# Kernel optimization log

Hardware: AMD Instinct MI355X
Metric: run time of the kernel (lower is better)

Reference implementation:

```python
import jax, jax.numpy as jnp
import numpy as np


def setup_inputs() -> dict:
    key = jax.random.key(0)
    kx, ky = jax.random.split(key)
    x = jax.random.normal(kx, (4, 8192, 3), dtype=jnp.float32)
    y = jax.random.normal(ky, (4, 8192, 3), dtype=jnp.float32)
    return {"x": x, "y": y}


def _chamfer(x, y):
    # x: [B, N, D], y: [B, M, D]
    x2 = jnp.sum(x * x, axis=-1)                      # [B, N]
    y2 = jnp.sum(y * y, axis=-1)                      # [B, M]
    xy = jnp.einsum("bnd,bmd->bnm", x, y)             # [B, N, M]
    d2 = x2[:, :, None] + y2[:, None, :] - 2.0 * xy   # [B, N, M]
    d2 = jnp.maximum(d2, 0.0)
    cham_x = jnp.min(d2, axis=2).mean(axis=1)         # [B] min over M, mean over N
    cham_y = jnp.min(d2, axis=1).mean(axis=1)         # [B] min over N, mean over M
    return cham_x + cham_y                            # [B]


def reference(x, y):
    per_batch = _chamfer(x, y)
    return jnp.mean(per_batch)  # batch_reduction='mean'
```

## Files before the change

kernel.cpp:

```cpp
#include <hip/hip_runtime.h>


#define N_      8192
#define NQ      65536
#define FLT_BIG 3.0e38f

__global__ void zero_out_kernel(float* out) { *out = 0.0f; }

__global__ __launch_bounds__(256) void init_kernel(unsigned int* __restrict__ pmin)
{
    int i = blockIdx.x * 256 + threadIdx.x;
    ((uint4*)pmin)[i] = make_uint4(0x7F800000u, 0x7F800000u, 0x7F800000u, 0x7F800000u);
}


__global__ __launch_bounds__(512, 4) void chamfer_kernel(
    const float* __restrict__ xraw, const float* __restrict__ yraw,
    unsigned int* __restrict__ pmin)
{
    __shared__ float lds[10240];
    float4* rec4 = (float4*)lds;
    float*  red  = lds;
    float*  qn   = lds + 9216;

    const int tid  = threadIdx.x;
    const int lane = tid & 63;
    const int wave = __builtin_amdgcn_readfirstlane(tid >> 6);
    const int blk  = blockIdx.x;
    const int dir   = blk >> 8;
    const int batch = (blk >> 6) & 3;
    const int qg    = (blk >> 3) & 7;
    const int seg   = blk & 7;

    const float* qraw = dir ? yraw : xraw;
    const float* oraw = dir ? xraw : yraw;

    {
        int r = tid;
        const float2* p2 = (const float2*)(oraw + ((size_t)batch * N_ + seg * 1024 + 2 * r) * 3);
        float2 a = p2[0], b = p2[1], c = p2[2];
        float w0 = fmaf(a.x, a.x, fmaf(a.y, a.y, b.x * b.x));
        float w1 = fmaf(b.y, b.y, fmaf(c.x, c.x, c.y * c.y));
        rec4[2*r]   = make_float4(a.x, a.y, b.x, w0);
        rec4[2*r+1] = make_float4(b.y, c.x, c.y, w1);
    }

    const int qbase = batch * N_ + qg * 1024;
    float qx[16], qy[16], qz[16], acc[16];
    #pragma unroll
    for (int j = 0; j < 16; ++j) {
        int q = lane + 64 * j;
        const float* qp = qraw + (size_t)(qbase + q) * 3;
        float ax = qp[0], ay = qp[1], az = qp[2];
        qx[j] = -2.0f * ax; qy[j] = -2.0f * ay; qz[j] = -2.0f * az;
        if (wave == 0) qn[q] = fmaf(ax, ax, fmaf(ay, ay, az * az));
        acc[j] = FLT_BIG;
    }
    __syncthreads();

    const float4* rp = rec4 + wave * 128;
    #pragma unroll 2
    for (int k = 0; k < 64; ++k) {
        float4 u = rp[2*k];
        float4 v = rp[2*k+1];
        #pragma unroll
        for (int j = 0; j < 16; ++j) {
            float t0 = fmaf(qz[j], u.z, u.w);
            t0 = fmaf(qy[j], u.y, t0);
            t0 = fmaf(qx[j], u.x, t0);
            float t1 = fmaf(qz[j], v.z, v.w);
            t1 = fmaf(qy[j], v.y, t1);
            t1 = fmaf(qx[j], v.x, t1);
            acc[j] = fminf(acc[j], fminf(t0, t1));
        }
    }
    __syncthreads();

    #pragma unroll
    for (int j = 0; j < 16; ++j) red[(lane + 64 * j) * 9 + wave] = acc[j];
    __syncthreads();

    #pragma unroll
    for (int r2 = 0; r2 < 2; ++r2) {
        int q = r2 * 512 + tid;
        float m = red[q * 9];
        #pragma unroll
        for (int w = 1; w < 8; ++w) m = fminf(m, red[q * 9 + w]);
        float d2 = fmaxf(0.0f, qn[q] + m);
        atomicMin(&pmin[dir * 32768 + qbase + q], __float_as_uint(d2));
    }
}

__global__ __launch_bounds__(1024) void sum_kernel(
    const unsigned int* __restrict__ pmin, float* __restrict__ out)
{
    __shared__ float sred[16];
    const int tid = threadIdx.x;
    const float4* pv = (const float4*)pmin;
    float s = 0.0f;
    #pragma unroll
    for (int k = 0; k < 16; ++k) {
        float4 v = pv[k * 1024 + tid];
        s += v.x + v.y + v.z + v.w;
    }
    #pragma unroll
    for (int off = 32; off > 0; off >>= 1) s += __shfl_xor(s, off);
    if ((tid & 63) == 0) sred[tid >> 6] = s;
    __syncthreads();
    if (tid < 16) {
        float v = sred[tid];
        #pragma unroll
        for (int off = 8; off > 0; off >>= 1) v += __shfl_xor(v, off);
        if (tid == 0) *out = v * (1.0f / 32768.0f);
    }
}

__global__ __launch_bounds__(1024) void chamfer_raw_kernel(
    const float* __restrict__ xraw, const float* __restrict__ yraw,
    float* __restrict__ out)
{
    __shared__ float4 red4[16][64];
    const int tid  = threadIdx.x;
    const int wave = tid >> 6;
    const int lane = tid & 63;
    const int blk  = blockIdx.x;
    const bool xdir = (blk < 128);
    const int b    = (blk & 127) >> 5;
    const int qofs = (blk & 31) << 8;
    const float* qraw = xdir ? xraw : yraw;
    const float* oraw = xdir ? yraw : xraw;
    float qx0[4], qx1[4], qx2[4], acc[4];
    #pragma unroll
    for (int q = 0; q < 4; ++q) {
        int gq = b * N_ + qofs + lane*4 + q;
        qx0[q] = qraw[gq*3+0]; qx1[q] = qraw[gq*3+1]; qx2[q] = qraw[gq*3+2];
        acc[q] = FLT_BIG;
    }
    const float* opp = oraw + (size_t)(b * N_ + wave * 512) * 3;
    #pragma unroll 4
    for (int k = 0; k < 512; ++k) {
        float p0 = opp[k*3+0], p1 = opp[k*3+1], p2 = opp[k*3+2];
        float w  = fmaf(p0, p0, fmaf(p1, p1, p2*p2));
        #pragma unroll
        for (int q = 0; q < 4; ++q) {
            float dot = qx0[q]*p0 + qx1[q]*p1 + qx2[q]*p2;
            acc[q] = fminf(acc[q], fmaf(-2.0f, dot, w));
        }
    }
    red4[wave][lane] = make_float4(acc[0], acc[1], acc[2], acc[3]);
    __syncthreads();
    if (tid < 256) {
        const float* red = (const float*)red4;
        float m = red[tid];
        #pragma unroll
        for (int w = 1; w < 16; ++w) m = fminf(m, red[w*256 + tid]);
        int gq = b * N_ + qofs + tid;
        float ax = qraw[gq*3+0], ay = qraw[gq*3+1], az = qraw[gq*3+2];
        float d2 = fmaxf(0.0f, fmaf(ax,ax,fmaf(ay,ay,az*az)) + m);
        #pragma unroll
        for (int off = 32; off > 0; off >>= 1) d2 += __shfl_xor(d2, off);
        if ((tid & 63) == 0) atomicAdd(out, d2 * (1.0f / 32768.0f));
    }
}

extern "C" void kernel_launch(void* const* d_in, const int* in_sizes, int n_in,
                              void* d_out, int out_size, void* d_ws, size_t ws_size,
                              hipStream_t stream)
{
    const float* x = (const float*)d_in[0];
    const float* y = (const float*)d_in[1];
    float* out = (float*)d_out;

    const size_t need = (size_t)NQ * 4;
    if (ws_size >= need) {
        unsigned int* pmin = (unsigned int*)d_ws;
        init_kernel<<<64, 256, 0, stream>>>(pmin);
        chamfer_kernel<<<512, 512, 0, stream>>>(x, y, pmin);
        sum_kernel<<<1, 1024, 0, stream>>>(pmin, out);
    } else {
        zero_out_kernel<<<1, 1, 0, stream>>>(out);
        chamfer_raw_kernel<<<256, 1024, 0, stream>>>(x, y, out);
    }
}
```

Before: 100.4 us.

## Split query register tile into two halves with software-prefetched LDS sweep

Processes the 16 per-thread query points in two passes of 8, reloading query coordinates between passes, to cut register pressure. The inner LDS loop now prefetches the next record pair ahead of the compute. The reduction buffer is moved to a separate LDS region so the second pass can be written without a sync, which raises LDS use per block. The cost is reading the opponent records from LDS twice and doing two global query loads instead of one.

```diff
diff --git a/kernel.cpp b/kernel.cpp
--- a/kernel.cpp
+++ b/kernel.cpp
@@ -13,15 +13,34 @@
     ((uint4*)pmin)[i] = make_uint4(0x7F800000u, 0x7F800000u, 0x7F800000u, 0x7F800000u);
 }
 
+static __device__ __forceinline__ void sweep8(
+    const float4* __restrict__ rp,
+    const float* qx, const float* qy, const float* qz, float* acc)
+{
+    float4 u = rp[0], v = rp[1];
+    #pragma unroll 2
+    for (int k = 0; k < 64; ++k) {
+        float4 un, vn;
+        if (k < 63) { un = rp[2*k+2]; vn = rp[2*k+3]; }
+        #pragma unroll
+        for (int j = 0; j < 8; ++j) {
+            float t0 = fmaf(qx[j], u.x, fmaf(qy[j], u.y, fmaf(qz[j], u.z, u.w)));
+            float t1 = fmaf(qx[j], v.x, fmaf(qy[j], v.y, fmaf(qz[j], v.z, v.w)));
+            acc[j] = fminf(acc[j], fminf(t0, t1));
+        }
+        u = un; v = vn;
+    }
+}
+
 
 __global__ __launch_bounds__(512, 4) void chamfer_kernel(
     const float* __restrict__ xraw, const float* __restrict__ yraw,
     unsigned int* __restrict__ pmin)
 {
-    __shared__ float lds[10240];
+    __shared__ float lds[14336];
     float4* rec4 = (float4*)lds;
-    float*  red  = lds;
-    float*  qn   = lds + 9216;
+    float*  red  = lds + 4096;
+    float*  qn   = lds + 13312;
 
     const int tid  = threadIdx.x;
     const int lane = tid & 63;
@@ -46,38 +65,39 @@
     }
 
     const int qbase = batch * N_ + qg * 1024;
-    float qx[16], qy[16], qz[16], acc[16];
-    #pragma unroll
-    for (int j = 0; j < 16; ++j) {
+    const float4* rp = rec4 + wave * 128;
+
+    float qx[8], qy[8], qz[8], accA[8], accB[8];
+
+    #pragma unroll
+    for (int j = 0; j < 8; ++j) {
         int q = lane + 64 * j;
         const float* qp = qraw + (size_t)(qbase + q) * 3;
         float ax = qp[0], ay = qp[1], az = qp[2];
         qx[j] = -2.0f * ax; qy[j] = -2.0f * ay; qz[j] = -2.0f * az;
         if (wave == 0) qn[q] = fmaf(ax, ax, fmaf(ay, ay, az * az));
-        acc[j] = FLT_BIG;
-    }
-    __syncthreads();
-
-    const float4* rp = rec4 + wave * 128;
-    #pragma unroll 2
-    for (int k = 0; k < 64; ++k) {
-        float4 u = rp[2*k];
-        float4 v = rp[2*k+1];
-        #pragma unroll
-        for (int j = 0; j < 16; ++j) {
-            float t0 = fmaf(qz[j], u.z, u.w);
-            t0 = fmaf(qy[j], u.y, t0);
-            t0 = fmaf(qx[j], u.x, t0);
-            float t1 = fmaf(qz[j], v.z, v.w);
-            t1 = fmaf(qy[j], v.y, t1);
-            t1 = fmaf(qx[j], v.x, t1);
-            acc[j] = fminf(acc[j], fminf(t0, t1));
-        }
-    }
-    __syncthreads();
-
-    #pragma unroll
-    for (int j = 0; j < 16; ++j) red[(lane + 64 * j) * 9 + wave] = acc[j];
+        accA[j] = FLT_BIG;
+    }
+    __syncthreads();
+
+    sweep8(rp, qx, qy, qz, accA);
+
+    #pragma unroll
+    for (int j = 0; j < 8; ++j) {
+        int q = lane + 64 * (j + 8);
+        const float* qp = qraw + (size_t)(qbase + q) * 3;
+        float ax = qp[0], ay = qp[1], az = qp[2];
+        qx[j] = -2.0f * ax; qy[j] = -2.0f * ay; qz[j] = -2.0f * az;
+        if (wave == 0) qn[q] = fmaf(ax, ax, fmaf(ay, ay, az * az));
+        accB[j] = FLT_BIG;
+    }
+    sweep8(rp, qx, qy, qz, accB);
+
+    #pragma unroll
+    for (int j = 0; j < 8; ++j) {
+        red[(lane + 64 * j) * 9 + wave]       = accA[j];
+        red[(lane + 64 * (j + 8)) * 9 + wave] = accB[j];
+    }
     __syncthreads();
 
     #pragma unroll
```

Result: slower. 104.5 us (+4.1%).
